# Kernel tuning notes

Measured on AMD Instinct MI355X. Metric: run time of the kernel, lower is better.

Reference implementation:

```python
import jax, jax.numpy as jnp
import numpy as np

N = 50000          # number of input/output nodes (M == N since out_features=None)
E = 1_600_000      # total neighbor entries (avg degree 32)
C_IN = 64
HID = 128
C_OUT = 64


def setup_inputs() -> dict:
    key = jax.random.key(0)
    k1, k2, k3, k4, k5 = jax.random.split(key, 5)
    in_features = jax.random.normal(k1, (N, C_IN), dtype=jnp.float32)
    # MLP params: Linear(2C->HID), GELU, Linear(HID->C_OUT)
    W1 = jax.random.normal(k2, (2 * C_IN, HID), dtype=jnp.float32) * (1.0 / np.sqrt(2 * C_IN))
    b1 = jnp.zeros((HID,), dtype=jnp.float32)
    W2 = jax.random.normal(k3, (HID, C_OUT), dtype=jnp.float32) * (1.0 / np.sqrt(HID))
    b2 = jnp.zeros((C_OUT,), dtype=jnp.float32)
    neighbors_index = jax.random.randint(k4, (E,), 0, N, dtype=jnp.int64)
    # row_splits: sorted, starts at 0, ends at E (CSR-style ragged offsets)
    inner = jnp.sort(jax.random.randint(k5, (N - 1,), 0, E, dtype=jnp.int64))
    neighbors_row_splits = jnp.concatenate(
        [jnp.zeros((1,), jnp.int64), inner, jnp.full((1,), E, jnp.int64)])
    return {
        "in_features": in_features,
        "W1": W1, "b1": b1, "W2": W2, "b2": b2,
        "neighbors_index": neighbors_index,
        "neighbors_row_splits": neighbors_row_splits,
    }


def reference(in_features, W1, b1, W2, b2, neighbors_index, neighbors_row_splits):
    rs = neighbors_row_splits
    counts = rs[1:] - rs[:-1]                                  # [M] num_reps per row
    # segment id of each edge: row i owns edges [rs[i], rs[i+1])
    seg_ids = jnp.searchsorted(rs[1:], jnp.arange(E), side="right")  # [E]

    rep_features = in_features[neighbors_index]                # gather neighbors [E, C]
    self_features = in_features[seg_ids]                       # repeat_interleave  [E, C]
    agg = jnp.concatenate([rep_features, self_features], axis=1)  # [E, 2C]

    h = jax.nn.gelu(agg @ W1 + b1, approximate=False)          # torch GELU = exact erf
    msg = h @ W2 + b2                                          # [E, C_out]

    summed = jax.ops.segment_sum(msg, seg_ids, num_segments=N)  # [M, C_out]
    denom = jnp.maximum(counts, 1).astype(msg.dtype)[:, None]
    return summed / denom                                       # mean reduction
```

## Files before the change

### kernel.cpp

```cpp
#include <hip/hip_runtime.h>
#include <hip/hip_bf16.h>
#include <math.h>

#define C_IN  64
#define HID   128
#define C_OUT 64

typedef __attribute__((ext_vector_type(8))) short s16x8;
typedef __attribute__((ext_vector_type(4))) float f32x4;
typedef __attribute__((ext_vector_type(2))) float f32x2;

__device__ __forceinline__ f32x2 gelu2(f32x2 x) {
    f32x2 t  = x * x;
    f32x2 p  = t * 0.10294455f + 2.30211462f;
    f32x2 xp = x * p;
    f32x2 E;
    E.x = __builtin_amdgcn_exp2f(xp.x);
    E.y = __builtin_amdgcn_exp2f(xp.y);
    f32x2 Ep = E + 1.0f;
    f32x2 r;
    r.x = __builtin_amdgcn_rcpf(Ep.x);
    r.y = __builtin_amdgcn_rcpf(Ep.y);
    return x - x * r;
}

__device__ __forceinline__ float4 fma4(float s, float4 w, float4 acc) {
    acc.x = fmaf(s, w.x, acc.x); acc.y = fmaf(s, w.y, acc.y);
    acc.z = fmaf(s, w.z, acc.z); acc.w = fmaf(s, w.w, acc.w);
    return acc;
}

__device__ __forceinline__ unsigned pk_bf16(float lo, float hi) {
    union { __hip_bfloat162 v; unsigned u; } cv;
    cv.v = __float22bfloat162_rn(make_float2(lo, hi));
    return cv.u;
}
__device__ __forceinline__ f32x2 unpk2(unsigned p) {
    union { unsigned u; float f; } lo, hi;
    lo.u = p << 16; hi.u = p & 0xffff0000u;
    f32x2 v; v.x = lo.f; v.y = hi.f; return v;
}

#define K1_NODES 64

__global__ __launch_bounds__(512, 2) void precompute_ab(
    const float* __restrict__ X, const float* __restrict__ W1,
    const float* __restrict__ b1, const float* __restrict__ W2,
    unsigned* __restrict__ A16, float* __restrict__ B,
    unsigned short* __restrict__ W2T, int N)
{
    __shared__ float W1s[2 * C_IN * HID];
    __shared__ float xs[K1_NODES * C_IN];
    int tid = threadIdx.x;

    for (int i = tid; i < (2 * C_IN * HID) / 4; i += 512)
        ((float4*)W1s)[i] = ((const float4*)W1)[i];

    int base = blockIdx.x * K1_NODES;
    int nLoc = min(K1_NODES, N - base);
    for (int i = tid; i < nLoc * (C_IN / 4); i += 512)
        ((float4*)xs)[i] = ((const float4*)(X + (size_t)base * C_IN))[i];

    if (blockIdx.x == 0) {
        for (int i = tid; i < C_OUT * HID; i += 512) {
            int c = i >> 7, k = i & (HID - 1);
            W2T[i] = (unsigned short)pk_bf16(W2[k * C_OUT + c], 0.f);
        }
    }
    __syncthreads();

    int quad = (tid & 31) * 4;
    int slot = tid >> 5;
    int s0   = slot * 4;
    if (s0 >= nLoc) return;

    float4 a0 = {}, a1 = {}, a2 = {}, a3 = {};
    float4 b0 = {}, b1r = {}, b2r = {}, b3 = {};

    const float* xr0 = xs + (s0 + 0) * C_IN;
    const float* xr1 = xs + (s0 + 1) * C_IN;
    const float* xr2 = xs + (s0 + 2) * C_IN;
    const float* xr3 = xs + (s0 + 3) * C_IN;

#define K1STEP(c, CMP)                                                      \
    do {                                                                    \
        float4 wa = *(const float4*)&W1s[(c) * HID + quad];                 \
        float4 wb = *(const float4*)&W1s[((c) + C_IN) * HID + quad];        \
        a0 = fma4(xv0.CMP, wa, a0); b0  = fma4(xv0.CMP, wb, b0);            \
        a1 = fma4(xv1.CMP, wa, a1); b1r = fma4(xv1.CMP, wb, b1r);           \
        a2 = fma4(xv2.CMP, wa, a2); b2r = fma4(xv2.CMP, wb, b2r);           \
        a3 = fma4(xv3.CMP, wa, a3); b3  = fma4(xv3.CMP, wb, b3);            \
    } while (0)

#pragma unroll 1
    for (int c4 = 0; c4 < C_IN; c4 += 4) {
        float4 xv0 = *(const float4*)&xr0[c4];
        float4 xv1 = *(const float4*)&xr1[c4];
        float4 xv2 = *(const float4*)&xr2[c4];
        float4 xv3 = *(const float4*)&xr3[c4];
        K1STEP(c4 + 0, x);
        K1STEP(c4 + 1, y);
        K1STEP(c4 + 2, z);
        K1STEP(c4 + 3, w);
    }
#undef K1STEP

    float4 bb = *(const float4*)(b1 + quad);
    b0.x += bb.x;  b0.y += bb.y;  b0.z += bb.z;  b0.w += bb.w;
    b1r.x += bb.x; b1r.y += bb.y; b1r.z += bb.z; b1r.w += bb.w;
    b2r.x += bb.x; b2r.y += bb.y; b2r.z += bb.z; b2r.w += bb.w;
    b3.x += bb.x;  b3.y += bb.y;  b3.z += bb.z;  b3.w += bb.w;

    int adw = (base + s0) * (HID / 2) + (quad >> 1);
    size_t boff = (size_t)(base + s0) * HID + quad;
    if (s0 + 0 < nLoc) {
        uint2 u = { pk_bf16(a0.x, a0.y), pk_bf16(a0.z, a0.w) };
        *(uint2*)(A16 + adw) = u;              *(float4*)(B + boff) = b0;
    }
    if (s0 + 1 < nLoc) {
        uint2 u = { pk_bf16(a1.x, a1.y), pk_bf16(a1.z, a1.w) };
        *(uint2*)(A16 + adw + HID / 2) = u;    *(float4*)(B + boff + HID) = b1r;
    }
    if (s0 + 2 < nLoc) {
        uint2 u = { pk_bf16(a2.x, a2.y), pk_bf16(a2.z, a2.w) };
        *(uint2*)(A16 + adw + HID) = u;        *(float4*)(B + boff + 2 * HID) = b2r;
    }
    if (s0 + 3 < nLoc) {
        uint2 u = { pk_bf16(a3.x, a3.y), pk_bf16(a3.z, a3.w) };
        *(uint2*)(A16 + adw + 3 * (HID / 2)) = u; *(float4*)(B + boff + 3 * HID) = b3;
    }
}

#define EA_WAVES 2

#define EA_ISSUE(P0,P1,P2,P3, g) do { int _s8 = ((g) << 3) + half;            \
    int _i0 = __shfl(idx, _s8);                                               \
    int _i1 = __shfl(idx, _s8 + 2);                                           \
    int _i2 = __shfl(idx, _s8 + 4);                                           \
    int _i3 = __shfl(idx, _s8 + 6);                                           \
    P0 = *(const uint2*)(A8 + ((((unsigned)_i0) << 8) | lb));                 \
    P1 = *(const uint2*)(A8 + ((((unsigned)_i1) << 8) | lb));                 \
    P2 = *(const uint2*)(A8 + ((((unsigned)_i2) << 8) | lb));                 \
    P3 = *(const uint2*)(A8 + ((((unsigned)_i3) << 8) | lb));                 \
} while (0)

#define EA_PROC1(P) do {                                                      \
    acc01 += gelu2(unpk2(P.x) + bb01);                                        \
    acc23 += gelu2(unpk2(P.y) + bb23); } while (0)

#define EA_PROC1M(P, p) do {                                                  \
    float _mk = ((((p) << 1) + half) < m) ? 1.f : 0.f;                        \
    acc01 += gelu2(unpk2(P.x) + bb01) * _mk;                                  \
    acc23 += gelu2(unpk2(P.y) + bb23) * _mk; } while (0)

#define EA_PROCG(P0,P1,P2,P3, g) do {                                         \
    if ((((g) + 1) << 3) <= m) { EA_PROC1(P0); EA_PROC1(P1);                  \
                                 EA_PROC1(P2); EA_PROC1(P3); }                \
    else { int _p = (g) << 2;                                                 \
           EA_PROC1M(P0, _p);                                                 \
           if (((_p + 1) << 1) < m) EA_PROC1M(P1, _p + 1);                    \
           if (((_p + 2) << 1) < m) EA_PROC1M(P2, _p + 2);                    \
           if (((_p + 3) << 1) < m) EA_PROC1M(P3, _p + 3); } } while (0)

__global__ __launch_bounds__(128) void edge_agg(
    const unsigned* __restrict__ A16, const float* __restrict__ B,
    const int* __restrict__ nbr, const int* __restrict__ rs,
    unsigned* __restrict__ Hout, int N, int E, int G)
{
    int wave = threadIdx.x >> 6, lane = threadIdx.x & 63;
    int half = lane >> 5, l5 = lane & 31;
    const char* A8 = (const char*)A16;
    unsigned lb = (unsigned)(l5 << 3);
    int b = blockIdx.x;

    int t0 = (int)(((long long)E * b) / G);
    int r0, r1;
    {
        int lo = 0, hi = N;
        while (lo < hi) { int mm = (lo + hi) >> 1; if (rs[mm] < t0) lo = mm + 1; else hi = mm; }
        r0 = lo;
    }
    if (b == G - 1) r1 = N;
    else {
        int t1 = (int)(((long long)E * (b + 1)) / G);
        int lo = r0, hi = N;
        while (lo < hi) { int mm = (lo + hi) >> 1; if (rs[mm] < t1) lo = mm + 1; else hi = mm; }
        r1 = lo;
    }

    for (int row = r0 + wave; row < r1; row += EA_WAVES) {
        int s = rs[row], e = rs[row + 1];
        int cnt = e - s;

        float4 bb4 = *(const float4*)(B + (size_t)row * HID + l5 * 4);
        f32x2 bb01, bb23;
        bb01.x = bb4.x; bb01.y = bb4.y; bb23.x = bb4.z; bb23.y = bb4.w;
        f32x2 acc01 = {0.f, 0.f}, acc23 = {0.f, 0.f};

        for (int cs = s; cs < e; cs += 64) {
            int m = min(64, e - cs);
            int idx = nbr[cs + min(lane, m - 1)];
            int ng = (m + 7) >> 3;

            uint2 A0, A1, A2, A3, B0, B1, B2, B3;

            EA_ISSUE(A0, A1, A2, A3, 0);
            int g = 0;
            for (;;) {
                if (g + 1 < ng) { EA_ISSUE(B0, B1, B2, B3, g + 1);
                                  EA_PROCG(A0, A1, A2, A3, g); ++g; }
                else            { EA_PROCG(A0, A1, A2, A3, g); break; }
                if (g + 1 < ng) { EA_ISSUE(A0, A1, A2, A3, g + 1);
                                  EA_PROCG(B0, B1, B2, B3, g); ++g; }
                else            { EA_PROCG(B0, B1, B2, B3, g); break; }
            }
        }

        acc01.x += __shfl_xor(acc01.x, 32);
        acc01.y += __shfl_xor(acc01.y, 32);
        acc23.x += __shfl_xor(acc23.x, 32);
        acc23.y += __shfl_xor(acc23.y, 32);

        if (half == 0) {
            float sc = (cnt > 0) ? 1.f / (float)cnt : 0.f;
            uint2 o = { pk_bf16(acc01.x * sc, acc01.y * sc),
                        pk_bf16(acc23.x * sc, acc23.y * sc) };
            ((uint2*)(Hout + (size_t)row * (HID / 2)))[l5] = o;
        }
    }
}

#undef EA_ISSUE
#undef EA_PROC1
#undef EA_PROC1M
#undef EA_PROCG

__global__ __launch_bounds__(256) void h_w2_mfma(
    const unsigned short* __restrict__ H, const unsigned short* __restrict__ W2T,
    const float* __restrict__ b2, const int* __restrict__ rs,
    float* __restrict__ out, int N)
{
    int wave = threadIdx.x >> 6, lane = threadIdx.x & 63;
    int base = (blockIdx.x * 4 + wave) * 16;
    if (base >= N) return;

    int r16 = lane & 15;
    int kg  = lane >> 4;

    const unsigned short* hrow = H + (size_t)(base + r16) * HID + kg * 8;
    const unsigned short* wc0  = W2T + (size_t)(0 * 16 + r16) * HID + kg * 8;
    const unsigned short* wc1  = W2T + (size_t)(1 * 16 + r16) * HID + kg * 8;
    const unsigned short* wc2  = W2T + (size_t)(2 * 16 + r16) * HID + kg * 8;
    const unsigned short* wc3  = W2T + (size_t)(3 * 16 + r16) * HID + kg * 8;

    f32x4 acc0 = {0.f, 0.f, 0.f, 0.f};
    f32x4 acc1 = acc0, acc2 = acc0, acc3 = acc0;

#pragma unroll
    for (int kk = 0; kk < 4; ++kk) {
        s16x8 a  = *(const s16x8*)(hrow + kk * 32);
        s16x8 f0 = *(const s16x8*)(wc0 + kk * 32);
        s16x8 f1 = *(const s16x8*)(wc1 + kk * 32);
        s16x8 f2 = *(const s16x8*)(wc2 + kk * 32);
        s16x8 f3 = *(const s16x8*)(wc3 + kk * 32);
        acc0 = __builtin_amdgcn_mfma_f32_16x16x32_bf16(a, f0, acc0, 0, 0, 0);
        acc1 = __builtin_amdgcn_mfma_f32_16x16x32_bf16(a, f1, acc1, 0, 0, 0);
        acc2 = __builtin_amdgcn_mfma_f32_16x16x32_bf16(a, f2, acc2, 0, 0, 0);
        acc3 = __builtin_amdgcn_mfma_f32_16x16x32_bf16(a, f3, acc3, 0, 0, 0);
    }

    float bia0 = b2[r16], bia1 = b2[16 + r16], bia2 = b2[32 + r16], bia3 = b2[48 + r16];

#pragma unroll
    for (int r = 0; r < 4; ++r) {
        int row = base + kg * 4 + r;
        if (row < N) {
            float mmk = (rs[row + 1] > rs[row]) ? 1.f : 0.f;
            float* o = out + (size_t)row * C_OUT;
            o[r16]      = mmk * (acc0[r] + bia0);
            o[16 + r16] = mmk * (acc1[r] + bia1);
            o[32 + r16] = mmk * (acc2[r] + bia2);
            o[48 + r16] = mmk * (acc3[r] + bia3);
        }
    }
}

extern "C" void kernel_launch(void* const* d_in, const int* in_sizes, int n_in,
                              void* d_out, int out_size, void* d_ws, size_t ws_size,
                              hipStream_t stream) {
    const float* X  = (const float*)d_in[0];
    const float* W1 = (const float*)d_in[1];
    const float* b1 = (const float*)d_in[2];
    const float* W2 = (const float*)d_in[3];
    const float* b2 = (const float*)d_in[4];
    const int*   nbr = (const int*)d_in[5];
    const int*   rs  = (const int*)d_in[6];
    float* outp = (float*)d_out;

    int N = in_sizes[6] - 1;
    int E = in_sizes[5];

    unsigned*       A16  = (unsigned*)d_ws;
    float*          Bbuf = (float*)(A16 + (size_t)N * (HID / 2));
    unsigned*       Hout = (unsigned*)(Bbuf + (size_t)N * HID);
    unsigned short* W2T  = (unsigned short*)(Hout + (size_t)N * (HID / 2));

    int g1 = (N + K1_NODES - 1) / K1_NODES;
    hipLaunchKernelGGL(precompute_ab, dim3(g1), dim3(512), 0, stream,
                       X, W1, b1, W2, A16, Bbuf, W2T, N);

    int G = 12288;
    hipLaunchKernelGGL(edge_agg, dim3(G), dim3(128), 0, stream,
                       A16, Bbuf, nbr, rs, Hout, N, E, G);

    int stripes = (N + 15) / 16;
    int g3 = (stripes + 3) / 4;
    hipLaunchKernelGGL(h_w2_mfma, dim3(g3), dim3(256), 0, stream,
                       (const unsigned short*)Hout, W2T, b2, rs, outp, N);
}
```

Baseline: 133.9 us.

## Precompute block row splits and software-pipeline edge gathers across rows

Moves the per-block binary searches over row_splits out of edge_agg and into precompute_ab, which writes the row range for each block to a workspace array. edge_agg now prefetches the next row's splits, bias vector and neighbor indices while it processes the current row, and deepens the gather pipeline from two to three register buffers. The aim is to hide the dependent-load latency at row and chunk boundaries. The cost is more live registers, which may reduce occupancy, plus a small dependency of edge_agg on extra work in the first kernel.

Result: faster. 129.3 us (-3.5%).

```diff
diff --git a/kernel.cpp b/kernel.cpp
--- a/kernel.cpp
+++ b/kernel.cpp
@@ -46,8 +46,10 @@
 __global__ __launch_bounds__(512, 2) void precompute_ab(
     const float* __restrict__ X, const float* __restrict__ W1,
     const float* __restrict__ b1, const float* __restrict__ W2,
+    const int* __restrict__ rs,
     unsigned* __restrict__ A16, float* __restrict__ B,
-    unsigned short* __restrict__ W2T, int N)
+    unsigned short* __restrict__ W2T, int* __restrict__ bsplit,
+    int N, int E, int G)
 {
     __shared__ float W1s[2 * C_IN * HID];
     __shared__ float xs[K1_NODES * C_IN];
@@ -67,6 +69,17 @@
             W2T[i] = (unsigned short)pk_bf16(W2[k * C_OUT + c], 0.f);
         }
     }
+
+    {
+        int gi = blockIdx.x * 512 + tid;
+        if (gi <= G) {
+            int t = (int)(((long long)E * gi) / G);
+            int lo = 0, hi = N;
+            while (lo < hi) { int mm = (lo + hi) >> 1; if (rs[mm] < t) lo = mm + 1; else hi = mm; }
+            bsplit[gi] = lo;
+        }
+    }
+
     __syncthreads();
 
     int quad = (tid & 31) * 4;
@@ -165,6 +178,7 @@
 __global__ __launch_bounds__(128) void edge_agg(
     const unsigned* __restrict__ A16, const float* __restrict__ B,
     const int* __restrict__ nbr, const int* __restrict__ rs,
+    const int* __restrict__ bsplit,
     unsigned* __restrict__ Hout, int N, int E, int G)
 {
     int wave = threadIdx.x >> 6, lane = threadIdx.x & 63;
@@ -173,47 +187,73 @@
     unsigned lb = (unsigned)(l5 << 3);
     int b = blockIdx.x;
 
-    int t0 = (int)(((long long)E * b) / G);
-    int r0, r1;
-    {
-        int lo = 0, hi = N;
-        while (lo < hi) { int mm = (lo + hi) >> 1; if (rs[mm] < t0) lo = mm + 1; else hi = mm; }
-        r0 = lo;
-    }
-    if (b == G - 1) r1 = N;
-    else {
-        int t1 = (int)(((long long)E * (b + 1)) / G);
-        int lo = r0, hi = N;
-        while (lo < hi) { int mm = (lo + hi) >> 1; if (rs[mm] < t1) lo = mm + 1; else hi = mm; }
-        r1 = lo;
-    }
-
-    for (int row = r0 + wave; row < r1; row += EA_WAVES) {
-        int s = rs[row], e = rs[row + 1];
+    int r0 = bsplit[b];
+    int r1 = (b == G - 1) ? N : bsplit[b + 1];
+
+    int row = r0 + wave;
+    if (row >= r1) return;
+
+    int s = rs[row], e = rs[row + 1];
+    float4 bb4 = *(const float4*)(B + (size_t)row * HID + l5 * 4);
+    int idx = 0;
+    if (e > s) { int mn = min(64, e - s); idx = nbr[s + min(lane, mn - 1)]; }
+
+    for (;;) {
         int cnt = e - s;
 
-        float4 bb4 = *(const float4*)(B + (size_t)row * HID + l5 * 4);
+        int nrow = row + EA_WAVES;
+        bool hasn = nrow < r1;
+        int sn = s, en = e;
+        float4 bbn = bb4;
+        if (hasn) {
+            sn = rs[nrow]; en = rs[nrow + 1];
+            bbn = *(const float4*)(B + (size_t)nrow * HID + l5 * 4);
+        }
+
         f32x2 bb01, bb23;
         bb01.x = bb4.x; bb01.y = bb4.y; bb23.x = bb4.z; bb23.y = bb4.w;
         f32x2 acc01 = {0.f, 0.f}, acc23 = {0.f, 0.f};
 
-        for (int cs = s; cs < e; cs += 64) {
-            int m = min(64, e - cs);
-            int idx = nbr[cs + min(lane, m - 1)];
-            int ng = (m + 7) >> 3;
-
-            uint2 A0, A1, A2, A3, B0, B1, B2, B3;
-
-            EA_ISSUE(A0, A1, A2, A3, 0);
-            int g = 0;
+        if (cnt > 0) {
+            int cs = s;
             for (;;) {
-                if (g + 1 < ng) { EA_ISSUE(B0, B1, B2, B3, g + 1);
-                                  EA_PROCG(A0, A1, A2, A3, g); ++g; }
-                else            { EA_PROCG(A0, A1, A2, A3, g); break; }
-                if (g + 1 < ng) { EA_ISSUE(A0, A1, A2, A3, g + 1);
-                                  EA_PROCG(B0, B1, B2, B3, g); ++g; }
-                else            { EA_PROCG(B0, B1, B2, B3, g); break; }
+                int m = min(64, e - cs);
+                int ng = (m + 7) >> 3;
+
+                uint2 A0, A1, A2, A3, B0, B1, B2, B3, C0, C1, C2, C3;
+                EA_ISSUE(A0, A1, A2, A3, 0);
+                if (ng > 1) EA_ISSUE(B0, B1, B2, B3, 1);
+
+                int ncs = cs + 64;
+                int idx_next = idx;
+                if (ncs < e) {
+                    int mn = min(64, e - ncs);
+                    idx_next = nbr[ncs + min(lane, mn - 1)];
+                } else if (hasn && en > sn) {
+                    int mn = min(64, en - sn);
+                    idx_next = nbr[sn + min(lane, mn - 1)];
+                }
+
+                int g = 0;
+                for (;;) {
+                    if (g + 2 < ng) EA_ISSUE(C0, C1, C2, C3, g + 2);
+                    EA_PROCG(A0, A1, A2, A3, g);
+                    if (++g >= ng) break;
+                    if (g + 2 < ng) EA_ISSUE(A0, A1, A2, A3, g + 2);
+                    EA_PROCG(B0, B1, B2, B3, g);
+                    if (++g >= ng) break;
+                    if (g + 2 < ng) EA_ISSUE(B0, B1, B2, B3, g + 2);
+                    EA_PROCG(C0, C1, C2, C3, g);
+                    if (++g >= ng) break;
+                }
+
+                idx = idx_next;
+                if (ncs >= e) break;
+                cs = ncs;
             }
+        } else if (hasn && en > sn) {
+            int mn = min(64, en - sn);
+            idx = nbr[sn + min(lane, mn - 1)];
         }
 
         acc01.x += __shfl_xor(acc01.x, 32);
@@ -227,6 +267,9 @@
                         pk_bf16(acc23.x * sc, acc23.y * sc) };
             ((uint2*)(Hout + (size_t)row * (HID / 2)))[l5] = o;
         }
+
+        if (!hasn) break;
+        row = nrow; s = sn; e = en; bb4 = bbn;
     }
 }
 
@@ -300,18 +343,20 @@
     int N = in_sizes[6] - 1;
     int E = in_sizes[5];
 
+    int G = 12288;
+
     unsigned*       A16  = (unsigned*)d_ws;
     float*          Bbuf = (float*)(A16 + (size_t)N * (HID / 2));
     unsigned*       Hout = (unsigned*)(Bbuf + (size_t)N * HID);
     unsigned short* W2T  = (unsigned short*)(Hout + (size_t)N * (HID / 2));
+    int*            bsplit = (int*)(W2T + C_OUT * HID);
 
     int g1 = (N + K1_NODES - 1) / K1_NODES;
     hipLaunchKernelGGL(precompute_ab, dim3(g1), dim3(512), 0, stream,
-                       X, W1, b1, W2, A16, Bbuf, W2T, N);
-
-    int G = 12288;
+                       X, W1, b1, W2, rs, A16, Bbuf, W2T, bsplit, N, E, G);
+
     hipLaunchKernelGGL(edge_agg, dim3(G), dim3(128), 0, stream,
-                       A16, Bbuf, nbr, rs, Hout, N, E, G);
+                       A16, Bbuf, nbr, rs, bsplit, Hout, N, E, G);
 
     int stripes = (N + 15) / 16;
     int g3 = (stripes + 3) / 4;
```

## Stage neighbor gathers into LDS with async global_load_lds triple-buffered pipeline

Applied to the files above, without the earlier changes.

Rewrites edge_agg as a single-wave block that walks rows in 32-edge chunks and gathers the neighbor A rows into double-buffered LDS with global_load_lds. Metadata for upcoming chunks (indices and bias rows) is prefetched, and explicit vmcnt waits overlap the gathers with the GELU accumulation. Per-block row split points are now computed once by binary search in precompute_ab rather than in every edge block. The hand-counted vmcnt waits, the dummy store and the fixed pipeline depth make correctness and scheduling fragile, and one wave per block lowers per-block parallelism.

New measurement: 161.6 us. +20.7%, slower.

```diff
diff --git a/kernel.cpp b/kernel.cpp
--- a/kernel.cpp
+++ b/kernel.cpp
@@ -5,10 +5,15 @@
 #define C_IN  64
 #define HID   128
 #define C_OUT 64
+#define K1_NODES 64
+#define EA_G  6144
 
 typedef __attribute__((ext_vector_type(8))) short s16x8;
 typedef __attribute__((ext_vector_type(4))) float f32x4;
 typedef __attribute__((ext_vector_type(2))) float f32x2;
+
+typedef const __attribute__((address_space(1))) unsigned g1u32;
+typedef __attribute__((address_space(3))) unsigned l3u32;
 
 __device__ __forceinline__ f32x2 gelu2(f32x2 x) {
     f32x2 t  = x * x;
@@ -41,13 +46,13 @@
     f32x2 v; v.x = lo.f; v.y = hi.f; return v;
 }
 
-#define K1_NODES 64
-
 __global__ __launch_bounds__(512, 2) void precompute_ab(
     const float* __restrict__ X, const float* __restrict__ W1,
     const float* __restrict__ b1, const float* __restrict__ W2,
+    const int* __restrict__ rs,
     unsigned* __restrict__ A16, float* __restrict__ B,
-    unsigned short* __restrict__ W2T, int N)
+    unsigned short* __restrict__ W2T, int* __restrict__ bsplit,
+    int N, int E, int G)
 {
     __shared__ float W1s[2 * C_IN * HID];
     __shared__ float xs[K1_NODES * C_IN];
@@ -67,6 +72,17 @@
             W2T[i] = (unsigned short)pk_bf16(W2[k * C_OUT + c], 0.f);
         }
     }
+
+    {
+        int gi = blockIdx.x * 512 + tid;
+        if (gi <= G) {
+            int t = (int)(((long long)E * gi) / G);
+            int lo = 0, hi = N;
+            while (lo < hi) { int mm = (lo + hi) >> 1; if (rs[mm] < t) lo = mm + 1; else hi = mm; }
+            bsplit[gi] = lo;
+        }
+    }
+
     __syncthreads();
 
     int quad = (tid & 31) * 4;
@@ -131,109 +147,171 @@
     }
 }
 
-#define EA_WAVES 2
-
-#define EA_ISSUE(P0,P1,P2,P3, g) do { int _s8 = ((g) << 3) + half;            \
-    int _i0 = __shfl(idx, _s8);                                               \
-    int _i1 = __shfl(idx, _s8 + 2);                                           \
-    int _i2 = __shfl(idx, _s8 + 4);                                           \
-    int _i3 = __shfl(idx, _s8 + 6);                                           \
-    P0 = *(const uint2*)(A8 + ((((unsigned)_i0) << 8) | lb));                 \
-    P1 = *(const uint2*)(A8 + ((((unsigned)_i1) << 8) | lb));                 \
-    P2 = *(const uint2*)(A8 + ((((unsigned)_i2) << 8) | lb));                 \
-    P3 = *(const uint2*)(A8 + ((((unsigned)_i3) << 8) | lb));                 \
+#define WAITVM(N) do { asm volatile("s_waitcnt vmcnt(" #N ")" ::: "memory");  \
+                       __builtin_amdgcn_sched_barrier(0); } while (0)
+#define VMFENCE() asm volatile("" ::: "memory")
+
+#define EA_ADV() do {                                                         \
+    if (srow >= r1) { dn_row = -1; dn_pos = 0; dn_len = 0; dn_cnt = 1; dn_first = 0; } \
+    else {                                                                    \
+        dn_row = srow; dn_pos = spos; dn_cnt = e0 - sS;                       \
+        dn_first = (spos == sS) ? 1 : 0;                                      \
+        int _rem = e0 - spos; dn_len = _rem < 32 ? _rem : 32;                 \
+        spos += dn_len;                                                       \
+        if (spos >= e0) {                                                     \
+            ++srow; sS = e0; e0 = e1; spos = sS;                              \
+            int _ni = srow + 2; _ni = _ni < N ? _ni : N;                      \
+            e1 = rs[__builtin_amdgcn_readfirstlane(_ni)];                     \
+        }                                                                     \
+    } } while (0)
+
+#define EA_META(DROW, DPOS, DLEN, IDXR, BBR) do {                             \
+    int _cl = (DLEN) > 0 ? (DLEN) - 1 : 0;                                    \
+    int _li = (DPOS) + (lane < _cl ? lane : _cl);                             \
+    _li = _li < E - 1 ? _li : E - 1; _li = _li > 0 ? _li : 0;                 \
+    IDXR = nbr[_li];                                                          \
+    int _br = (DROW) >= 0 ? (DROW) : 0;                                       \
+    BBR = *(const float4*)(B + ((size_t)_br << 7) + (l5 << 2));               \
 } while (0)
 
-#define EA_PROC1(P) do {                                                      \
+#define EA_STAGE8(SLOTP, LEN, IDXR) do {                                      \
+    int _cl = (LEN) > 0 ? (LEN) - 1 : 0;                                      \
+    char* _sp = (SLOTP);                                                      \
+    _Pragma("unroll")                                                         \
+    for (int _g = 0; _g < 8; ++_g) {                                          \
+        int _sh = (_g << 2) + (lane >> 4); _sh = _sh < _cl ? _sh : _cl;       \
+        int _ie = __shfl((IDXR), _sh);                                        \
+        const char* _gp = A8 + (((size_t)(unsigned)_ie) << 8) + ((lane & 15) << 4); \
+        __builtin_amdgcn_global_load_lds((g1u32*)_gp,                         \
+                                         (l3u32*)(_sp + (_g << 10)), 16, 0, 0); \
+    } } while (0)
+
+#define EA_LDE(SLOT, G, T) (*(const uint2*)((SLOT) + ((((G)<<3)+((T)<<1)+half)<<8) + (l5<<3)))
+
+#define EA_PAIR(P) do {                                                       \
     acc01 += gelu2(unpk2(P.x) + bb01);                                        \
     acc23 += gelu2(unpk2(P.y) + bb23); } while (0)
 
-#define EA_PROC1M(P, p) do {                                                  \
-    float _mk = ((((p) << 1) + half) < m) ? 1.f : 0.f;                        \
+#define EA_PAIRM(P, EB) do {                                                  \
+    float _mk = ((EB) + half < m) ? 1.f : 0.f;                                \
     acc01 += gelu2(unpk2(P.x) + bb01) * _mk;                                  \
     acc23 += gelu2(unpk2(P.y) + bb23) * _mk; } while (0)
 
-#define EA_PROCG(P0,P1,P2,P3, g) do {                                         \
-    if ((((g) + 1) << 3) <= m) { EA_PROC1(P0); EA_PROC1(P1);                  \
-                                 EA_PROC1(P2); EA_PROC1(P3); }                \
-    else { int _p = (g) << 2;                                                 \
-           EA_PROC1M(P0, _p);                                                 \
-           if (((_p + 1) << 1) < m) EA_PROC1M(P1, _p + 1);                    \
-           if (((_p + 2) << 1) < m) EA_PROC1M(P2, _p + 2);                    \
-           if (((_p + 3) << 1) < m) EA_PROC1M(P3, _p + 3); } } while (0)
-
-__global__ __launch_bounds__(128) void edge_agg(
+#define EA_GRP(SLOT, G) do {                                                  \
+    if (((G) << 3) < m) {                                                     \
+        uint2 _P0 = EA_LDE(SLOT, G, 0), _P1 = EA_LDE(SLOT, G, 1);             \
+        uint2 _P2 = EA_LDE(SLOT, G, 2), _P3 = EA_LDE(SLOT, G, 3);             \
+        if ((((G) + 1) << 3) <= m) {                                          \
+            EA_PAIR(_P0); EA_PAIR(_P1); EA_PAIR(_P2); EA_PAIR(_P3);           \
+        } else { int _eb = (G) << 3;                                          \
+            EA_PAIRM(_P0, _eb);                                               \
+            if (_eb + 2 < m) EA_PAIRM(_P1, _eb + 2);                          \
+            if (_eb + 4 < m) EA_PAIRM(_P2, _eb + 4);                          \
+            if (_eb + 6 < m) EA_PAIRM(_P3, _eb + 6);                          \
+        }                                                                     \
+    } } while (0)
+
+__global__ __launch_bounds__(64, 2) void edge_agg(
     const unsigned* __restrict__ A16, const float* __restrict__ B,
     const int* __restrict__ nbr, const int* __restrict__ rs,
-    unsigned* __restrict__ Hout, int N, int E, int G)
+    const int* __restrict__ bsplit,
+    unsigned* __restrict__ Hout, unsigned* __restrict__ dump,
+    int N, int E, int G)
 {
-    int wave = threadIdx.x >> 6, lane = threadIdx.x & 63;
+    __shared__ __align__(1024) char lds0[8192];
+    __shared__ __align__(1024) char lds1[8192];
+
+    int lane = threadIdx.x;
     int half = lane >> 5, l5 = lane & 31;
     const char* A8 = (const char*)A16;
-    unsigned lb = (unsigned)(l5 << 3);
     int b = blockIdx.x;
 
-    int t0 = (int)(((long long)E * b) / G);
-    int r0, r1;
-    {
-        int lo = 0, hi = N;
-        while (lo < hi) { int mm = (lo + hi) >> 1; if (rs[mm] < t0) lo = mm + 1; else hi = mm; }
-        r0 = lo;
-    }
-    if (b == G - 1) r1 = N;
-    else {
-        int t1 = (int)(((long long)E * (b + 1)) / G);
-        int lo = r0, hi = N;
-        while (lo < hi) { int mm = (lo + hi) >> 1; if (rs[mm] < t1) lo = mm + 1; else hi = mm; }
-        r1 = lo;
-    }
-
-    for (int row = r0 + wave; row < r1; row += EA_WAVES) {
-        int s = rs[row], e = rs[row + 1];
-        int cnt = e - s;
-
-        float4 bb4 = *(const float4*)(B + (size_t)row * HID + l5 * 4);
+    int r0 = bsplit[b];
+    int r1 = (b == G - 1) ? N : bsplit[b + 1];
+    if (r0 >= r1) return;
+
+    int srow = r0;
+    int sS = rs[r0];
+    int e0 = rs[r0 + 1];
+    int ni0 = r0 + 2; ni0 = ni0 < N ? ni0 : N;
+    int e1 = rs[ni0];
+    int spos = sS;
+
+    int dn_row, dn_pos, dn_len, dn_cnt, dn_first;
+    EA_ADV();
+    int d0_row = dn_row, d0_pos = dn_pos, d0_len = dn_len, d0_cnt = dn_cnt, d0_first = dn_first;
+    EA_ADV();
+    int d1_row = dn_row, d1_pos = dn_pos, d1_len = dn_len, d1_cnt = dn_cnt, d1_first = dn_first;
+    EA_ADV();
+    int d2_row = dn_row, d2_pos = dn_pos, d2_len = dn_len, d2_cnt = dn_cnt, d2_first = dn_first;
+
+    int idxT0, idxT1, idxS, idxA;
+    float4 bb0, bb1, bb2;
+
+    EA_META(d0_row, d0_pos, d0_len, idxT0, bb0);
+    EA_META(d1_row, d1_pos, d1_len, idxT1, bb1);
+    WAITVM(0);
+    EA_STAGE8(lds0, d0_len, idxT0);
+    VMFENCE();
+    if (half == 0) { uint2 z = {0u, 0u}; ((uint2*)dump)[l5] = z; }
+    VMFENCE();
+    EA_META(d2_row, d2_pos, d2_len, idxS, bb2);
+    VMFENCE();
+    EA_STAGE8(lds1, d1_len, idxT1);
+
+    char* slotC = lds0;
+    char* slotS = lds1;
+    f32x2 acc01 = {0.f, 0.f}, acc23 = {0.f, 0.f};
+
+    for (;;) {
+        if (d0_row < 0) break;
+
+        WAITVM(11);
+        if (d0_first) { acc01.x = 0.f; acc01.y = 0.f; acc23.x = 0.f; acc23.y = 0.f; }
         f32x2 bb01, bb23;
-        bb01.x = bb4.x; bb01.y = bb4.y; bb23.x = bb4.z; bb23.y = bb4.w;
-        f32x2 acc01 = {0.f, 0.f}, acc23 = {0.f, 0.f};
-
-        for (int cs = s; cs < e; cs += 64) {
-            int m = min(64, e - cs);
-            int idx = nbr[cs + min(lane, m - 1)];
-            int ng = (m + 7) >> 3;
-
-            uint2 A0, A1, A2, A3, B0, B1, B2, B3;
-
-            EA_ISSUE(A0, A1, A2, A3, 0);
-            int g = 0;
-            for (;;) {
-                if (g + 1 < ng) { EA_ISSUE(B0, B1, B2, B3, g + 1);
-                                  EA_PROCG(A0, A1, A2, A3, g); ++g; }
-                else            { EA_PROCG(A0, A1, A2, A3, g); break; }
-                if (g + 1 < ng) { EA_ISSUE(A0, A1, A2, A3, g + 1);
-                                  EA_PROCG(B0, B1, B2, B3, g); ++g; }
-                else            { EA_PROCG(B0, B1, B2, B3, g); break; }
-            }
+        bb01.x = bb0.x; bb01.y = bb0.y; bb23.x = bb0.z; bb23.y = bb0.w;
+        int m = d0_len;
+        EA_GRP(slotC, 0);
+        EA_GRP(slotC, 1);
+        EA_GRP(slotC, 2);
+        EA_GRP(slotC, 3);
+
+        f32x2 r01 = acc01, r23 = acc23;
+        r01.x += __shfl_xor(r01.x, 32);
+        r01.y += __shfl_xor(r01.y, 32);
+        r23.x += __shfl_xor(r23.x, 32);
+        r23.y += __shfl_xor(r23.y, 32);
+        VMFENCE();
+        if (half == 0) {
+            float sc = (d0_cnt > 0) ? 1.f / (float)d0_cnt : 0.f;
+            uint2 o = { pk_bf16(r01.x * sc, r01.y * sc),
+                        pk_bf16(r23.x * sc, r23.y * sc) };
+            ((uint2*)(Hout + ((size_t)d0_row << 6)))[l5] = o;
         }
-
-        acc01.x += __shfl_xor(acc01.x, 32);
-        acc01.y += __shfl_xor(acc01.y, 32);
-        acc23.x += __shfl_xor(acc23.x, 32);
-        acc23.y += __shfl_xor(acc23.y, 32);
-
-        if (half == 0) {
-            float sc = (cnt > 0) ? 1.f / (float)cnt : 0.f;
-            uint2 o = { pk_bf16(acc01.x * sc, acc01.y * sc),
-                        pk_bf16(acc23.x * sc, acc23.y * sc) };
-            ((uint2*)(Hout + (size_t)row * (HID / 2)))[l5] = o;
-        }
-    }
-}
-
-#undef EA_ISSUE
-#undef EA_PROC1
-#undef EA_PROC1M
-#undef EA_PROCG
+        VMFENCE();
+
+        WAITVM(9);
+        EA_ADV();
+        idxA = idxS;
+        bb0 = bb1; bb1 = bb2;
+        EA_META(dn_row, dn_pos, dn_len, idxS, bb2);
+        VMFENCE();
+        EA_STAGE8(slotC, d2_len, idxA);
+
+        d0_row = d1_row; d0_pos = d1_pos; d0_len = d1_len; d0_cnt = d1_cnt; d0_first = d1_first;
+        d1_row = d2_row; d1_pos = d2_pos; d1_len = d2_len; d1_cnt = d2_cnt; d1_first = d2_first;
+        d2_row = dn_row; d2_pos = dn_pos; d2_len = dn_len; d2_cnt = dn_cnt; d2_first = dn_first;
+        char* tmp = slotC; slotC = slotS; slotS = tmp;
+    }
+}
+
+#undef EA_ADV
+#undef EA_META
+#undef EA_STAGE8
+#undef EA_LDE
+#undef EA_PAIR
+#undef EA_PAIRM
+#undef EA_GRP
 
 __global__ __launch_bounds__(256) void h_w2_mfma(
     const unsigned short* __restrict__ H, const unsigned short* __restrict__ W2T,
@@ -273,10 +351,10 @@
 
 #pragma unroll
     for (int r = 0; r < 4; ++r) {
-        int row = base + kg * 4 + r;
-        if (row < N) {
-            float mmk = (rs[row + 1] > rs[row]) ? 1.f : 0.f;
-            float* o = out + (size_t)row * C_OUT;
+        int rowi = base + kg * 4 + r;
+        if (rowi < N) {
+            float mmk = (rs[rowi + 1] > rs[rowi]) ? 1.f : 0.f;
+            float* o = out + (size_t)rowi * C_OUT;
             o[r16]      = mmk * (acc0[r] + bia0);
             o[16 + r16] = mmk * (acc1[r] + bia1);
             o[32 + r16] = mmk * (acc2[r] + bia2);
@@ -300,18 +378,21 @@
     int N = in_sizes[6] - 1;
     int E = in_sizes[5];
 
+    int G = EA_G;
+
     unsigned*       A16  = (unsigned*)d_ws;
     float*          Bbuf = (float*)(A16 + (size_t)N * (HID / 2));
     unsigned*       Hout = (unsigned*)(Bbuf + (size_t)N * HID);
     unsigned short* W2T  = (unsigned short*)(Hout + (size_t)N * (HID / 2));
+    int*            bsplit = (int*)(W2T + C_OUT * HID);
+    unsigned*       dump = (unsigned*)(bsplit + (G + 2));
 
     int g1 = (N + K1_NODES - 1) / K1_NODES;
     hipLaunchKernelGGL(precompute_ab, dim3(g1), dim3(512), 0, stream,
-                       X, W1, b1, W2, A16, Bbuf, W2T, N);
-
-    int G = 12288;
-    hipLaunchKernelGGL(edge_agg, dim3(G), dim3(128), 0, stream,
-                       A16, Bbuf, nbr, rs, Hout, N, E, G);
+                       X, W1, b1, W2, rs, A16, Bbuf, W2T, bsplit, N, E, G);
+
+    hipLaunchKernelGGL(edge_agg, dim3(G), dim3(64), 0, stream,
+                       A16, Bbuf, nbr, rs, bsplit, Hout, dump, N, E, G);
 
     int stripes = (N + 15) / 16;
     int g3 = (stripes + 3) / 4;
```
